# Kernel optimization log

Measured on AMD Instinct MI355X. Metric: run time of the kernel, lower is better.

Reference implementation:

```python
import jax, jax.numpy as jnp
import numpy as np

OUT = 3      # pooled output size (fmap_size//4 = 14//4 = 3)
RATIO = 2    # roi_align sampling ratio (fixed; torchvision adaptive ratio for 14/3 bins is 2)
P = 20       # num_persons


def _bilinear(fm, y, x):
    # fm: [C,H,W]; y,x broadcastable coordinate grids. torchvision aligned=False semantics.
    C, H, W = fm.shape
    y, x = jnp.broadcast_arrays(y, x)
    valid = (y > -1.0) & (y < H) & (x > -1.0) & (x < W)
    y = jnp.clip(y, 0.0, H - 1.0)
    x = jnp.clip(x, 0.0, W - 1.0)
    y0 = jnp.floor(y).astype(jnp.int32)
    x0 = jnp.floor(x).astype(jnp.int32)
    y1 = jnp.minimum(y0 + 1, H - 1)
    x1 = jnp.minimum(x0 + 1, W - 1)
    ly = y - y0
    lx = x - x0
    hy = 1.0 - ly
    hx = 1.0 - lx
    v00 = fm[:, y0, x0]
    v01 = fm[:, y0, x1]
    v10 = fm[:, y1, x0]
    v11 = fm[:, y1, x1]
    val = hy * hx * v00 + hy * lx * v01 + ly * hx * v10 + ly * lx * v11
    return jnp.where(valid, val, 0.0)  # [C, ...]


def _roi_align_one(fm, box):
    # fm: [C,H,W], box: [4] = (x1,y1,x2,y2) in feature-map coords -> [C,OUT,OUT]
    x1, y1, x2, y2 = box
    bw = (x2 - x1) / OUT
    bh = (y2 - y1) / OUT
    off = (jnp.arange(OUT * RATIO, dtype=fm.dtype) + 0.5) / RATIO  # bin-unit offsets
    xs = x1 + off * bw
    ys = y1 + off * bh
    vals = _bilinear(fm, ys[:, None], xs[None, :])  # [C, OUT*RATIO, OUT*RATIO]
    C = fm.shape[0]
    return vals.reshape(C, OUT, RATIO, OUT, RATIO).mean(axis=(2, 4))


def setup_inputs() -> dict:
    key = jax.random.key(0)
    ks = jax.random.split(key, 8)
    B, N, NB, C, FS = 128, 8, 27, 1024, 14
    fmap = jax.random.normal(ks[0], (B, C, FS, FS), jnp.float32)
    # boxes in feature-map coordinates with x1<x2, y1<y2
    lo = jax.random.uniform(ks[1], (B, N, 2), jnp.float32) * 10.0
    ext = 2.0 + jax.random.uniform(ks[2], (B, N, 2), jnp.float32) * 4.0
    hi = jnp.minimum(lo + ext, float(FS))
    boxes = jnp.concatenate([lo, hi], axis=-1)  # [B,N,4] (x1,y1,x2,y2)
    # unique person ids per frame (scatter target indices)
    pids = jax.vmap(lambda k: jax.random.permutation(k, P)[:N])(jax.random.split(ks[3], B)).astype(jnp.int32)
    w1 = jax.random.normal(ks[4], (512, C), jnp.float32) * 0.02
    w2 = jax.random.normal(ks[5], (256, 512), jnp.float32) * 0.05
    fc1_w = jax.random.normal(ks[6], (1024, 256 * OUT * OUT), jnp.float32) * 0.02
    fc1_b = jnp.zeros((1024,), jnp.float32)
    fc2_w = jax.random.normal(ks[7], (27, 1024), jnp.float32) * 0.02
    fc2_b = jnp.zeros((27,), jnp.float32)
    return {"fmap": fmap, "boxes": boxes, "pids": pids, "w1": w1, "w2": w2,
            "fc1_w": fc1_w, "fc1_b": fc1_b, "fc2_w": fc2_w, "fc2_b": fc2_b}


def _forward(fmap, boxes, pids, w1, w2, fc1_w, fc1_b, fc2_w, fc2_b):
    B, N = boxes.shape[:2]
    # per-image, per-box ROI align: [B,N,C,3,3]
    roi = jax.vmap(jax.vmap(_roi_align_one, in_axes=(None, 0)), in_axes=(0, 0))(fmap, boxes)
    # behavior_conv: two bias-free 1x1 convs (no nonlinearity between)
    h = jnp.einsum('bnchw,oc->bnohw', roi, w1)
    h = jnp.einsum('bnchw,oc->bnohw', h, w2)  # [B,N,256,3,3]
    feat = h.reshape(B, N, -1)                # [B,N,2304]
    bidx = jnp.broadcast_to(jnp.arange(B)[:, None], (B, N))
    # scatter into behavior_tensor keyed by person id (unique pids per frame -> well-defined)
    bt = jnp.zeros((B, P, feat.shape[-1]), feat.dtype).at[bidx, pids].set(feat)
    mean_b = bt.mean(axis=0)                  # [P,2304] mean over batch
    cur = bt[bidx, pids]                      # [B,N,2304]
    diff = mean_b[pids] - cur
    # behavior_fc (dropout is identity at inference)
    h1 = jax.nn.relu(jnp.einsum('bnd,hd->bnh', diff, fc1_w) + fc1_b)
    return jnp.einsum('bnh,oh->bno', h1, fc2_w) + fc2_b  # [B,N,num_behaviors]


def reference(fmap, boxes, pids, w1, w2, fc1_w, fc1_b, fc2_w, fc2_b):
    # fmap is detached and roi_align runs under no_grad in the original
    return _forward(jax.lax.stop_gradient(fmap), jax.lax.stop_gradient(boxes), pids,
                    w1, w2, fc1_w, fc1_b, fc2_w, fc2_b)
```

## Files before the change

### kernel.cpp

```cpp
#include <hip/hip_runtime.h>
#include <hip/hip_bf16.h>
#include <cstddef>
#include <cstdint>

#define B_   128
#define N_   8
#define C_   1024
#define FS_  14
#define POS_ 196
#define P_   20
#define HWC_ 9
#define CMID_ 256
#define FEATD_ 2304
#define H1_  1024
#define O_   27

typedef __attribute__((ext_vector_type(8))) short bf16x8;
typedef __attribute__((ext_vector_type(4))) float f32x4;

__device__ __forceinline__ void gld16(const void* g, void* l) {
    __builtin_amdgcn_global_load_lds(
        (const __attribute__((address_space(1))) unsigned int*)g,
        (__attribute__((address_space(3))) unsigned int*)l, 16, 0, 0);
}

__global__ __launch_bounds__(256) void wcombine_split_kernel(
    const float* __restrict__ w1,
    const float* __restrict__ w2,
    float* __restrict__ wpart)
{
    const int tid = threadIdx.x;
    const int tx = tid & 15, ty = tid >> 4;
    const int c0 = blockIdx.x * 64;
    const int o0 = blockIdx.y * 64;
    const int kb = blockIdx.z * 64;
    __shared__ __align__(16) float As[16][68];
    __shared__ __align__(16) float Bs[16][68];
    float acc[4][4] = {};
    for (int k0 = kb; k0 < kb + 64; k0 += 16) {
        for (int i = tid; i < 64 * 16; i += 256) {
            int k = i & 15, m = i >> 4;
            As[k][m] = w2[(size_t)(o0 + m) * 512 + k0 + k];
        }
        for (int i = tid; i < 64 * 16; i += 256) {
            int n = i & 63, k = i >> 6;
            Bs[k][n] = w1[(size_t)(k0 + k) * 1024 + c0 + n];
        }
        __syncthreads();
        #pragma unroll
        for (int k = 0; k < 16; ++k) {
            float4 a = *(const float4*)&As[k][ty * 4];
            float4 b = *(const float4*)&Bs[k][tx * 4];
            float av[4] = {a.x, a.y, a.z, a.w};
            float bv[4] = {b.x, b.y, b.z, b.w};
            #pragma unroll
            for (int i = 0; i < 4; ++i)
                #pragma unroll
                for (int j = 0; j < 4; ++j)
                    acc[i][j] += av[i] * bv[j];
        }
        __syncthreads();
    }
    float* dst = wpart + (size_t)blockIdx.z * (256 * 1024);
    for (int i = 0; i < 4; ++i) {
        float4 v = make_float4(acc[i][0], acc[i][1], acc[i][2], acc[i][3]);
        *(float4*)&dst[(size_t)(o0 + ty * 4 + i) * 1024 + c0 + tx * 4] = v;
    }
}

__global__ __launch_bounds__(256) void wc_reduce_kernel(
    const float* __restrict__ wpart, __hip_bfloat16* __restrict__ Wc)
{
    int idx = blockIdx.x * 256 + threadIdx.x;
    float s = 0.f;
    #pragma unroll
    for (int z = 0; z < 8; ++z) s += wpart[(size_t)z * (256 * 1024) + idx];
    Wc[idx] = __float2bfloat16(s);
}

#define SSTR_  232
#define AROWS_ 72
#define BOFF_  (AROWS_ * SSTR_)
#define PSTR_  72
#define POFF_  (BOFF_ + 64 * SSTR_)
#define NCHUNK_ 4
struct bf4s { __hip_bfloat162 lo, hi; };
__global__ __launch_bounds__(256, 2) void poolmix_kernel(
    const float* __restrict__ fmap,
    const float* __restrict__ boxes,
    const __hip_bfloat16* __restrict__ Wc,
    float* __restrict__ featp)
{
    const int cq = blockIdx.x;
    const int b  = blockIdx.y;
    const int tid = threadIdx.x;
    const int wave = tid >> 6, lane = tid & 63;
    const int m16 = lane & 15, quad = lane >> 4;
    __shared__ __align__(16) __hip_bfloat16 Ls[POFF_ + AROWS_ * PSTR_];

    if (tid < AROWS_) {
        const int m = tid;
        const int n = m / 9, cell = m - n * 9;
        const int chh = cell / 3, cww = cell % 3;
        float4 bx = *(const float4*)(boxes + ((size_t)b * N_ + n) * 4);
        float bw = (bx.z - bx.x) * (1.0f / 3.0f);
        float bh = (bx.w - bx.y) * (1.0f / 3.0f);
        float ypro[FS_], xpro[FS_];
        #pragma unroll
        for (int k = 0; k < FS_; ++k) { ypro[k] = 0.f; xpro[k] = 0.f; }
        #pragma unroll
        for (int s = 0; s < 2; ++s) {
            float yy = bx.y + ((float)(2 * chh + s) + 0.5f) * 0.5f * bh;
            bool vy = (yy > -1.0f) && (yy < (float)FS_);
            float y = fminf(fmaxf(yy, 0.0f), (float)(FS_ - 1));
            int y0 = (int)floorf(y);
            int y1i = min(y0 + 1, FS_ - 1);
            float ly = y - (float)y0, hy = 1.0f - ly;
            float qy = vy ? 0.5f : 0.0f;
            float w0 = hy * qy, w1 = ly * qy;
            #pragma unroll
            for (int k = 0; k < FS_; ++k)
                ypro[k] += (k == y0 ? w0 : 0.f) + (k == y1i ? w1 : 0.f);
            float xx = bx.x + ((float)(2 * cww + s) + 0.5f) * 0.5f * bw;
            bool vx = (xx > -1.0f) && (xx < (float)FS_);
            float x = fminf(fmaxf(xx, 0.0f), (float)(FS_ - 1));
            int x0 = (int)floorf(x);
            int x1i = min(x0 + 1, FS_ - 1);
            float lx = x - (float)x0, hx = 1.0f - lx;
            float qx = vx ? 0.5f : 0.0f;
            float u0 = hx * qx, u1 = lx * qx;
            #pragma unroll
            for (int k = 0; k < FS_; ++k)
                xpro[k] += (k == x0 ? u0 : 0.f) + (k == x1i ? u1 : 0.f);
        }
        __hip_bfloat162* row2 = (__hip_bfloat162*)&Ls[m * SSTR_];
        #pragma unroll
        for (int p = 0; p < 98; ++p) {
            const int i0 = 2 * p, i1 = 2 * p + 1;
            __hip_bfloat162 t;
            t.x = __float2bfloat16(ypro[i0 / FS_] * xpro[i0 % FS_]);
            t.y = __float2bfloat16(ypro[i1 / FS_] * xpro[i1 % FS_]);
            row2[p] = t;
        }
        const __hip_bfloat16 z16 = __float2bfloat16(0.0f);
        #pragma unroll
        for (int p = 98; p < SSTR_ / 2; ++p) {
            __hip_bfloat162 t; t.x = z16; t.y = z16;
            row2[p] = t;
        }
    }
    for (int i = tid; i < 64 * 18; i += 256) {
        int r = i / 18, kd = i - r * 18;
        *(unsigned int*)&Ls[BOFF_ + r * SSTR_ + 196 + kd * 2] = 0;
    }
    const int cbase0 = cq * 256;
    {
        const float* src = fmap + ((size_t)b * C_ + cbase0) * POS_;
        #pragma unroll
        for (int it = 0; it < 13; ++it) {
            int i = tid + it * 256;
            if (i < 64 * 49) {
                int cr = i / 49, ch = i - cr * 49;
                float4 v = *(const float4*)(src + (size_t)cr * POS_ + ch * 4);
                bf4s t;
                t.lo.x = __float2bfloat16(v.x); t.lo.y = __float2bfloat16(v.y);
                t.hi.x = __float2bfloat16(v.z); t.hi.y = __float2bfloat16(v.w);
                *(bf4s*)&Ls[BOFF_ + cr * SSTR_ + ch * 4] = t;
            }
        }
    }

    f32x4 acc2[5][4];
    #pragma unroll
    for (int mt = 0; mt < 5; ++mt)
        #pragma unroll
        for (int nt = 0; nt < 4; ++nt)
            acc2[mt][nt] = (f32x4){0.f, 0.f, 0.f, 0.f};

    float4 vbuf[13];
    for (int c = 0; c < NCHUNK_; ++c) {
        __syncthreads();

        if (c < NCHUNK_ - 1) {
            const float* src = fmap + ((size_t)b * C_ + cbase0 + (c + 1) * 64) * POS_;
            #pragma unroll
            for (int it = 0; it < 13; ++it) {
                int i = tid + it * 256;
                if (i < 64 * 49) {
                    int cr = i / 49, ch = i - cr * 49;
                    vbuf[it] = *(const float4*)(src + (size_t)cr * POS_ + ch * 4);
                }
            }
        }

        f32x4 acc1[5];
        #pragma unroll
        for (int mt = 0; mt < 5; ++mt) acc1[mt] = (f32x4){0.f, 0.f, 0.f, 0.f};
        const int nrow = wave * 16 + m16;
        #pragma unroll
        for (int kk = 0; kk < 7; ++kk) {
            bf16x8 bfv = *(const bf16x8*)&Ls[BOFF_ + nrow * SSTR_ + kk * 32 + quad * 8];
            #pragma unroll
            for (int mt = 0; mt < 5; ++mt) {
                bf16x8 af = *(const bf16x8*)&Ls[(mt * 16 + m16) * SSTR_ + kk * 32 + quad * 8];
                acc1[mt] = __builtin_amdgcn_mfma_f32_16x16x32_bf16(af, bfv, acc1[mt], 0, 0, 0);
            }
        }
        #pragma unroll
        for (int mt = 0; mt < 5; ++mt) {
            #pragma unroll
            for (int g = 0; g < 4; ++g) {
                int cell = mt * 16 + quad * 4 + g;
                if (cell < AROWS_)
                    Ls[POFF_ + cell * PSTR_ + wave * 16 + m16] =
                        __float2bfloat16(acc1[mt][g]);
            }
        }
        __syncthreads();

        #pragma unroll
        for (int ks = 0; ks < 2; ++ks) {
            bf16x8 af[5];
            #pragma unroll
            for (int mt = 0; mt < 5; ++mt)
                af[mt] = *(const bf16x8*)&Ls[POFF_ + (mt * 16 + m16) * PSTR_ + ks * 32 + quad * 8];
            #pragma unroll
            for (int nt = 0; nt < 4; ++nt) {
                int n = wave * 64 + nt * 16 + m16;
                bf16x8 bfv = *(const bf16x8*)(Wc + (size_t)n * C_ + cbase0 + c * 64 + ks * 32 + quad * 8);
                #pragma unroll
                for (int mt = 0; mt < 5; ++mt)
                    acc2[mt][nt] = __builtin_amdgcn_mfma_f32_16x16x32_bf16(
                        af[mt], bfv, acc2[mt][nt], 0, 0, 0);
            }
        }

        if (c < NCHUNK_ - 1) {
            #pragma unroll
            for (int it = 0; it < 13; ++it) {
                int i = tid + it * 256;
                if (i < 64 * 49) {
                    int cr = i / 49, ch = i - cr * 49;
                    float4 v = vbuf[it];
                    bf4s t;
                    t.lo.x = __float2bfloat16(v.x); t.lo.y = __float2bfloat16(v.y);
                    t.hi.x = __float2bfloat16(v.z); t.hi.y = __float2bfloat16(v.w);
                    *(bf4s*)&Ls[BOFF_ + cr * SSTR_ + ch * 4] = t;
                }
            }
        }
    }

    float* dst = featp + (size_t)cq * ((size_t)128 * AROWS_ * 256);
    #pragma unroll
    for (int mt = 0; mt < 5; ++mt) {
        #pragma unroll
        for (int g = 0; g < 4; ++g) {
            int row = mt * 16 + quad * 4 + g;
            if (row < AROWS_) {
                #pragma unroll
                for (int nt = 0; nt < 4; ++nt)
                    dst[(size_t)(b * AROWS_ + row) * 256 + wave * 64 + nt * 16 + m16] =
                        acc2[mt][nt][g];
            }
        }
    }
}

__global__ __launch_bounds__(256, 4) void fc1_gemm_kernel(
    const __hip_bfloat16* __restrict__ A,
    const __hip_bfloat16* __restrict__ Bm,
    const float* __restrict__ bias,
    float* __restrict__ C)
{
    const int tid = threadIdx.x;
    const int wave = tid >> 6, lane = tid & 63;
    const int r0 = blockIdx.y * 32, n0 = blockIdx.x * 64;
    const int wm = (wave >> 1) * 16, wn = (wave & 1) * 32;
    const int m16 = lane & 15, quad = lane >> 4;
    const int K = FEATD_;
    __shared__ __align__(16) __hip_bfloat16 As[32 * 64];
    __shared__ __align__(16) __hip_bfloat16 Bs[64 * 64];

    f32x4 acc[2];
    acc[0] = (f32x4){0.f, 0.f, 0.f, 0.f};
    acc[1] = (f32x4){0.f, 0.f, 0.f, 0.f};

    const int qa = wave * 64 + lane;
    const int msA = qa >> 3, csA = (qa & 7) ^ (msA & 7);
    const int qb1 = qa + 256;
    const int msB1 = qb1 >> 3, csB1 = (qb1 & 7) ^ (msB1 & 7);
    const size_t rA  = (size_t)(r0 + msA)  * K + csA  * 8;
    const size_t rB0 = (size_t)(n0 + msA)  * K + csA  * 8;
    const size_t rB1 = (size_t)(n0 + msB1) * K + csB1 * 8;

    for (int k0 = 0; k0 < K; k0 += 64) {
        gld16(A  + rA  + k0, &As[wave * 512]);
        gld16(Bm + rB0 + k0, &Bs[wave * 512]);
        gld16(Bm + rB1 + k0, &Bs[2048 + wave * 512]);
        __syncthreads();
        #pragma unroll
        for (int ks = 0; ks < 2; ++ks) {
            bf16x8 af, bfv[2];
            int m = wm + m16;
            int cp = (ks * 4 + quad) ^ (m & 7);
            af = *(const bf16x8*)&As[(m * 8 + cp) * 8];
            #pragma unroll
            for (int t = 0; t < 2; ++t) {
                int n = wn + t * 16 + m16;
                int cq = (ks * 4 + quad) ^ (n & 7);
                bfv[t] = *(const bf16x8*)&Bs[(n * 8 + cq) * 8];
            }
            #pragma unroll
            for (int j = 0; j < 2; ++j)
                acc[j] = __builtin_amdgcn_mfma_f32_16x16x32_bf16(
                    af, bfv[j], acc[j], 0, 0, 0);
        }
        __syncthreads();
    }

    #pragma unroll
    for (int j = 0; j < 2; ++j) {
        int col = n0 + wn + j * 16 + m16;
        int rbase = r0 + wm + quad * 4;
        float bv = bias[col];
        #pragma unroll
        for (int g = 0; g < 4; ++g) {
            int r = rbase + g;
            float v = acc[j][g] + bv;
            C[(size_t)r * H1_ + col] = v > 0.f ? v : 0.f;
        }
    }
}

__global__ __launch_bounds__(256) void fc1w_perm_kernel(
    const float* __restrict__ src, __hip_bfloat16* __restrict__ dst)
{
    int h = blockIdx.x;
    int tid = threadIdx.x;
    __shared__ float buf[FEATD_];
    const float* s = src + (size_t)h * FEATD_;
    #pragma unroll
    for (int it = 0; it < 9; ++it)
        buf[it * 256 + tid] = s[it * 256 + tid];
    __syncthreads();
    __hip_bfloat16* d = dst + (size_t)h * FEATD_;
    #pragma unroll
    for (int it = 0; it < 9; ++it) {
        int dd = it * 256 + tid;
        d[dd] = __float2bfloat16(buf[tid * HWC_ + it]);
    }
}

__global__ __launch_bounds__(256) void meandiff_kernel(
    const float* __restrict__ featp, const int* __restrict__ pids,
    __hip_bfloat16* __restrict__ diff)
{
    const size_t PART = (size_t)(B_ * N_) * FEATD_;
    int p = blockIdx.x;
    int d = blockIdx.y * 256 + threadIdx.x;
    __shared__ int invs[B_];
    if (threadIdx.x < B_) {
        int bb = threadIdx.x;
        int v = -1;
        #pragma unroll
        for (int n = 0; n < N_; ++n)
            if (pids[bb * N_ + n] == p) v = n;
        invs[bb] = v;
    }
    __syncthreads();

    float acc = 0.0f;
    #pragma unroll 4
    for (int b = 0; b < B_; ++b) {
        int n = invs[b];
        if (n >= 0) {
            size_t idx = (size_t)(b * N_ + n) * FEATD_ + d;
            acc += (featp[idx] + featp[idx + PART]) +
                   (featp[idx + 2 * PART] + featp[idx + 3 * PART]);
        }
    }
    float mean = acc * (1.0f / (float)B_);
    #pragma unroll 4
    for (int b = 0; b < B_; ++b) {
        int n = invs[b];
        if (n >= 0) {
            size_t idx = (size_t)(b * N_ + n) * FEATD_ + d;
            float v = (featp[idx] + featp[idx + PART]) +
                      (featp[idx + 2 * PART] + featp[idx + 3 * PART]);
            diff[idx] = __float2bfloat16(mean - v);
        }
    }
}

__global__ __launch_bounds__(256) void fc2_kernel(
    const float* __restrict__ h1, const float* __restrict__ fc2_w,
    const float* __restrict__ fc2_b, float* __restrict__ out)
{
    int bn = blockIdx.x;
    int tid = threadIdx.x;
    __shared__ __align__(16) float row[H1_];
    __shared__ float partial[32][8];
    ((float4*)row)[tid] = ((const float4*)(h1 + (size_t)bn * H1_))[tid];
    __syncthreads();
    int o = tid >> 3, part = tid & 7;
    float acc = 0.0f;
    if (o < O_) {
        const float* wrow = fc2_w + (size_t)o * H1_ + part * 128;
        const float* hrow = row + part * 128;
        #pragma unroll 4
        for (int j = 0; j < 128; ++j) acc += hrow[j] * wrow[j];
    }
    partial[o][part] = acc;
    __syncthreads();
    if (part == 0 && o < O_) {
        float s = fc2_b[o];
        #pragma unroll
        for (int p = 0; p < 8; ++p) s += partial[o][p];
        out[(size_t)bn * O_ + o] = s;
    }
}

extern "C" void kernel_launch(void* const* d_in, const int* in_sizes, int n_in,
                              void* d_out, int out_size, void* d_ws, size_t ws_size,
                              hipStream_t stream) {
    const float* fmap  = (const float*)d_in[0];
    const float* boxes = (const float*)d_in[1];
    const int*   pids  = (const int*)  d_in[2];
    const float* w1    = (const float*)d_in[3];
    const float* w2    = (const float*)d_in[4];
    const float* fc1_w = (const float*)d_in[5];
    const float* fc1_b = (const float*)d_in[6];
    const float* fc2_w = (const float*)d_in[7];
    const float* fc2_b = (const float*)d_in[8];
    float* out = (float*)d_out;

    char* wsb = (char*)d_ws;
    __hip_bfloat16* Wc    = (__hip_bfloat16*)wsb;
    __hip_bfloat16* fc1wp = Wc + 256 * 1024;
    __hip_bfloat16* diffp = fc1wp + (size_t)H1_ * FEATD_;
    float* featp  = (float*)(diffp + (size_t)H1_ * FEATD_);
    float* h1     = featp + 4 * (size_t)(B_ * N_) * FEATD_;
    float* wpart  = h1 + (size_t)(B_ * N_) * H1_;

    hipLaunchKernelGGL(wcombine_split_kernel, dim3(16, 4, 8), dim3(256), 0, stream,
                       w1, w2, wpart);
    hipLaunchKernelGGL(wc_reduce_kernel, dim3(1024), dim3(256), 0, stream,
                       wpart, Wc);
    hipLaunchKernelGGL(poolmix_kernel, dim3(4, 128), dim3(256), 0, stream,
                       fmap, boxes, Wc, featp);
    hipLaunchKernelGGL(fc1w_perm_kernel, dim3(1024), dim3(256), 0, stream,
                       fc1_w, fc1wp);
    hipLaunchKernelGGL(meandiff_kernel, dim3(20, 9), dim3(256), 0, stream,
                       featp, pids, diffp);
    hipLaunchKernelGGL(fc1_gemm_kernel, dim3(16, 32), dim3(256), 0, stream,
                       diffp, fc1wp, fc1_b, h1);
    hipLaunchKernelGGL(fc2_kernel, dim3(1024), dim3(256), 0, stream,
                       h1, fc2_w, fc2_b, out);
}
```

Before: 296.1 us.

## Load fmap MFMA B-fragments directly into registers, bypassing LDS staging

The pooling-matrix GEMM now has each lane load its fmap row segment from global memory straight into registers in MFMA fragment layout. It converts these to bf16 in registers instead of staging the 64x196 chunk through shared memory. This removes the LDS writes and reads, the zero-padding pass and the shared buffer for fmap, and moves the barrier placement. In exchange, global loads are less coalesced (each lane reads 32-byte pieces of a row) and register pressure rises from the 13 prefetch float4s plus 7 converted fragments.

```diff
diff --git a/kernel.cpp b/kernel.cpp
--- a/kernel.cpp
+++ b/kernel.cpp
@@ -22,6 +22,11 @@
     __builtin_amdgcn_global_load_lds(
         (const __attribute__((address_space(1))) unsigned int*)g,
         (__attribute__((address_space(3))) unsigned int*)l, 16, 0, 0);
+}
+
+__device__ __forceinline__ short bfs(float f) {
+    __hip_bfloat16 h = __float2bfloat16(f);
+    return *(short*)&h;
 }
 
 __global__ __launch_bounds__(256) void wcombine_split_kernel(
@@ -80,11 +85,9 @@
 
 #define SSTR_  232
 #define AROWS_ 72
-#define BOFF_  (AROWS_ * SSTR_)
 #define PSTR_  72
-#define POFF_  (BOFF_ + 64 * SSTR_)
+#define POFF_  (AROWS_ * SSTR_)
 #define NCHUNK_ 4
-struct bf4s { __hip_bfloat162 lo, hi; };
 __global__ __launch_bounds__(256, 2) void poolmix_kernel(
     const float* __restrict__ fmap,
     const float* __restrict__ boxes,
@@ -97,6 +100,21 @@
     const int wave = tid >> 6, lane = tid & 63;
     const int m16 = lane & 15, quad = lane >> 4;
     __shared__ __align__(16) __hip_bfloat16 Ls[POFF_ + AROWS_ * PSTR_];
+
+    const int cbase0 = cq * 256;
+    const int nrow = wave * 16 + m16;
+    const float* frow0 = fmap + ((size_t)b * C_ + cbase0 + nrow) * POS_;
+
+    float4 pf[13];
+    {
+        const float* fr = frow0 + quad * 8;
+        #pragma unroll
+        for (int kk = 0; kk < 6; ++kk) {
+            pf[2 * kk]     = *(const float4*)(fr + kk * 32);
+            pf[2 * kk + 1] = *(const float4*)(fr + kk * 32 + 4);
+        }
+        if (quad == 0) pf[12] = *(const float4*)(frow0 + 192);
+    }
 
     if (tid < AROWS_) {
         const int m = tid;
@@ -149,26 +167,7 @@
             row2[p] = t;
         }
     }
-    for (int i = tid; i < 64 * 18; i += 256) {
-        int r = i / 18, kd = i - r * 18;
-        *(unsigned int*)&Ls[BOFF_ + r * SSTR_ + 196 + kd * 2] = 0;
-    }
-    const int cbase0 = cq * 256;
-    {
-        const float* src = fmap + ((size_t)b * C_ + cbase0) * POS_;
-        #pragma unroll
-        for (int it = 0; it < 13; ++it) {
-            int i = tid + it * 256;
-            if (i < 64 * 49) {
-                int cr = i / 49, ch = i - cr * 49;
-                float4 v = *(const float4*)(src + (size_t)cr * POS_ + ch * 4);
-                bf4s t;
-                t.lo.x = __float2bfloat16(v.x); t.lo.y = __float2bfloat16(v.y);
-                t.hi.x = __float2bfloat16(v.z); t.hi.y = __float2bfloat16(v.w);
-                *(bf4s*)&Ls[BOFF_ + cr * SSTR_ + ch * 4] = t;
-            }
-        }
-    }
+    __syncthreads();
 
     f32x4 acc2[5][4];
     #pragma unroll
@@ -177,35 +176,49 @@
         for (int nt = 0; nt < 4; ++nt)
             acc2[mt][nt] = (f32x4){0.f, 0.f, 0.f, 0.f};
 
-    float4 vbuf[13];
     for (int c = 0; c < NCHUNK_; ++c) {
-        __syncthreads();
+        bf16x8 bf[7];
+        #pragma unroll
+        for (int kk = 0; kk < 6; ++kk) {
+            float4 a = pf[2 * kk], bb = pf[2 * kk + 1];
+            bf16x8 r;
+            r[0] = bfs(a.x); r[1] = bfs(a.y); r[2] = bfs(a.z); r[3] = bfs(a.w);
+            r[4] = bfs(bb.x); r[5] = bfs(bb.y); r[6] = bfs(bb.z); r[7] = bfs(bb.w);
+            bf[kk] = r;
+        }
+        {
+            bf16x8 r = (bf16x8){0, 0, 0, 0, 0, 0, 0, 0};
+            if (quad == 0) {
+                float4 a = pf[12];
+                r[0] = bfs(a.x); r[1] = bfs(a.y); r[2] = bfs(a.z); r[3] = bfs(a.w);
+            }
+            bf[6] = r;
+        }
 
         if (c < NCHUNK_ - 1) {
-            const float* src = fmap + ((size_t)b * C_ + cbase0 + (c + 1) * 64) * POS_;
-            #pragma unroll
-            for (int it = 0; it < 13; ++it) {
-                int i = tid + it * 256;
-                if (i < 64 * 49) {
-                    int cr = i / 49, ch = i - cr * 49;
-                    vbuf[it] = *(const float4*)(src + (size_t)cr * POS_ + ch * 4);
-                }
-            }
+            const float* frow = frow0 + (size_t)((c + 1) * 64) * POS_;
+            const float* fr = frow + quad * 8;
+            #pragma unroll
+            for (int kk = 0; kk < 6; ++kk) {
+                pf[2 * kk]     = *(const float4*)(fr + kk * 32);
+                pf[2 * kk + 1] = *(const float4*)(fr + kk * 32 + 4);
+            }
+            if (quad == 0) pf[12] = *(const float4*)(frow + 192);
         }
 
         f32x4 acc1[5];
         #pragma unroll
         for (int mt = 0; mt < 5; ++mt) acc1[mt] = (f32x4){0.f, 0.f, 0.f, 0.f};
-        const int nrow = wave * 16 + m16;
         #pragma unroll
         for (int kk = 0; kk < 7; ++kk) {
-            bf16x8 bfv = *(const bf16x8*)&Ls[BOFF_ + nrow * SSTR_ + kk * 32 + quad * 8];
             #pragma unroll
             for (int mt = 0; mt < 5; ++mt) {
                 bf16x8 af = *(const bf16x8*)&Ls[(mt * 16 + m16) * SSTR_ + kk * 32 + quad * 8];
-                acc1[mt] = __builtin_amdgcn_mfma_f32_16x16x32_bf16(af, bfv, acc1[mt], 0, 0, 0);
-            }
-        }
+                acc1[mt] = __builtin_amdgcn_mfma_f32_16x16x32_bf16(af, bf[kk], acc1[mt], 0, 0, 0);
+            }
+        }
+        __syncthreads();
+
         #pragma unroll
         for (int mt = 0; mt < 5; ++mt) {
             #pragma unroll
@@ -232,21 +245,6 @@
                 for (int mt = 0; mt < 5; ++mt)
                     acc2[mt][nt] = __builtin_amdgcn_mfma_f32_16x16x32_bf16(
                         af[mt], bfv, acc2[mt][nt], 0, 0, 0);
-            }
-        }
-
-        if (c < NCHUNK_ - 1) {
-            #pragma unroll
-            for (int it = 0; it < 13; ++it) {
-                int i = tid + it * 256;
-                if (i < 64 * 49) {
-                    int cr = i / 49, ch = i - cr * 49;
-                    float4 v = vbuf[it];
-                    bf4s t;
-                    t.lo.x = __float2bfloat16(v.x); t.lo.y = __float2bfloat16(v.y);
-                    t.hi.x = __float2bfloat16(v.z); t.hi.y = __float2bfloat16(v.w);
-                    *(bf4s*)&Ls[BOFF_ + cr * SSTR_ + ch * 4] = t;
-                }
             }
         }
     }
```

Measured after the change: 293.4 us. Within noise of the previous version (-0.9%).
